# Kernel tuning notes

Measured on AMD Instinct MI355X. Metric: run time of the kernel, lower is better.

## Reference

```python
import jax, jax.numpy as jnp
import numpy as np

N_NODES = 50000
N_EDGES = 800000
D = 128


def setup_inputs() -> dict:
    key = jax.random.key(0)
    ks = jax.random.split(key, 8)
    s = 1.0 / np.sqrt(D)
    return {
        "x": jax.random.normal(ks[0], (N_NODES, D), dtype=jnp.float32),
        "edge_index": jax.random.randint(ks[1], (2, N_EDGES), 0, N_NODES, dtype=jnp.int32),
        "W0l": jax.random.normal(ks[2], (D, D), dtype=jnp.float32) * s,
        "b0l": jnp.zeros((D,), dtype=jnp.float32),
        "W0r": jax.random.normal(ks[3], (D, D), dtype=jnp.float32) * s,
        "W1l": jax.random.normal(ks[4], (D, D), dtype=jnp.float32) * s,
        "b1l": jnp.zeros((D,), dtype=jnp.float32),
        "W1r": jax.random.normal(ks[5], (D, D), dtype=jnp.float32) * s,
    }


def reference(x, edge_index, W0l, b0l, W0r, W1l, b1l, W1r):
    # Encoder(conv='sage', num_layers=2), eval mode (dropout = identity).
    src = edge_index[0]  # x_j gathered from source nodes
    dst = edge_index[1]  # aggregated at target nodes
    # in-degree for mean aggregation; isolated nodes get 0 aggregate (PyG mean)
    deg = jax.ops.segment_sum(jnp.ones_like(dst, dtype=x.dtype), dst, num_segments=N_NODES)
    inv_deg = jnp.where(deg > 0, 1.0 / jnp.maximum(deg, 1.0), 0.0)[:, None]

    def sage(h, Wl, bl, Wr):
        m = h @ Wl + bl                                        # lin_l
        agg = jax.ops.segment_sum(m[src], dst, num_segments=N_NODES) * inv_deg  # mean aggr
        return agg + h @ Wr                                    # + lin_r skip

    h = jax.nn.relu(sage(x, W0l, b0l, W0r))   # layer 0 + relu
    return sage(h, W1l, b1l, W1r)             # final layer
```

## Files before the change

kernel.cpp:

```cpp
#include <hip/hip_runtime.h>

#define N_NODES 50000
#define N_EDGES 800000
#define D 128
#define NBLK ((N_NODES + 255) / 256)
#define EPB 4096
#define CAP 8192
#define PCAP 8192

typedef __bf16 bf16x8 __attribute__((ext_vector_type(8)));
typedef short s16x8 __attribute__((ext_vector_type(8)));
typedef float f32x4 __attribute__((ext_vector_type(4)));
typedef float f32x2 __attribute__((ext_vector_type(2)));
typedef unsigned short u16;
typedef unsigned int u32;
typedef unsigned char u8;
typedef u32 u32x2 __attribute__((ext_vector_type(2)));
typedef u32 u32x4 __attribute__((ext_vector_type(4)));
typedef u16 u16x4 __attribute__((ext_vector_type(4)));

__device__ inline u16 f32_to_bf16(float f) {
    u32 u = __builtin_bit_cast(u32, f);
    u += 0x7fffu + ((u >> 16) & 1u);
    return (u16)(u >> 16);
}

__device__ inline f32x4 mfma16(s16x8 a, s16x8 b, f32x4 c) {
    return __builtin_amdgcn_mfma_f32_16x16x32_bf16(
        __builtin_bit_cast(bf16x8, a), __builtin_bit_cast(bf16x8, b), c, 0, 0, 0);
}

#define CAST_BLOCKS ((N_NODES * 16) / 256)
#define STAGE_BLOCKS ((N_EDGES + EPB - 1) / EPB)

__global__ __launch_bounds__(256) void prep_stage(
    const float* __restrict__ x, u16* __restrict__ xb, u16* __restrict__ hb,
    u8* __restrict__ xf8, u8* __restrict__ hf8,
    const float* __restrict__ W0l, const float* __restrict__ W0r,
    const float* __restrict__ W1l, const float* __restrict__ W1r,
    u16* __restrict__ Wp,
    const int* __restrict__ src, const int* __restrict__ dst,
    int* __restrict__ ccount, u32* __restrict__ staged) {
    __shared__ int hist[NBLK];
    __shared__ int base[NBLK];
    int t = threadIdx.x, b = blockIdx.x;
    if (b < CAST_BLOCKS) {
        int gid = b * 256 + t;
        const float* p = x + (size_t)gid * 8;
        f32x4 a = *(const f32x4*)p;
        f32x4 c = *(const f32x4*)(p + 4);
        u16 o[8];
#pragma unroll
        for (int j = 0; j < 4; j++) { o[j] = f32_to_bf16(a[j]); o[4 + j] = f32_to_bf16(c[j]); }
        *(s16x8*)(xb + (size_t)gid * 8) = *(const s16x8*)o;
        int p0 = __builtin_amdgcn_cvt_pk_fp8_f32(a.x, a.y, 0, false);
        int p1 = __builtin_amdgcn_cvt_pk_fp8_f32(a.z, a.w, 0, false);
        int p2 = __builtin_amdgcn_cvt_pk_fp8_f32(c.x, c.y, 0, false);
        int p3 = __builtin_amdgcn_cvt_pk_fp8_f32(c.z, c.w, 0, false);
        u32x2 w;
        w.x = (u32)(p0 & 0xffff) | ((u32)(p1 & 0xffff) << 16);
        w.y = (u32)(p2 & 0xffff) | ((u32)(p3 & 0xffff) << 16);
        *(u32x2*)(xf8 + (size_t)gid * 8) = w;
    } else if (b < CAST_BLOCKS + 32) {
        int gid = (b - CAST_BLOCKS) * 256 + t;
        int wsel = gid >> 11;
        int rem  = gid & 2047;
        int ct   = rem >> 8;
        int ks   = (rem >> 6) & 3;
        int lane = rem & 63;
        const float* W = (wsel == 0) ? W0l : (wsel == 1) ? W0r : (wsel == 2) ? W1l : W1r;
        int n  = ct * 16 + (lane & 15);
        int k0 = ks * 32 + (lane >> 4) * 8;
        u16 o[8];
#pragma unroll
        for (int j = 0; j < 8; j++) o[j] = f32_to_bf16(W[(k0 + j) * D + n]);
        u16* dp = Wp + wsel * 16384 + (size_t)((ct * 4 + ks) * 64 + lane) * 8;
        *(s16x8*)dp = *(const s16x8*)o;
    } else if (b < CAST_BLOCKS + 33) {
        if (t < 64)        ((u32*)(xb + (size_t)N_NODES * D))[t] = 0;
        else if (t < 128)  ((u32*)(hb + (size_t)N_NODES * D))[t - 64] = 0;
        else if (t < 160)  ((u32*)(xf8 + (size_t)N_NODES * D))[t - 128] = 0;
        else if (t < 192)  ((u32*)(hf8 + (size_t)N_NODES * D))[t - 160] = 0;
    } else {
        int sb = b - CAST_BLOCKS - 33;
        int bb = sb * EPB;
        if (t < NBLK) hist[t] = 0;
        __syncthreads();
        u32 pk[16]; int cb[16];
#pragma unroll
        for (int i = 0; i < 16; i++) {
            int e = bb + i * 256 + t;
            if (e < N_EDGES) {
                int sv = src[e], dv = dst[e];
                pk[i] = (u32)sv | ((u32)(dv & 255) << 16);
                cb[i] = dv >> 8;
                atomicAdd(&hist[cb[i]], 1);
            } else cb[i] = -1;
        }
        __syncthreads();
        if (t < NBLK) {
            int c = hist[t];
            if (c > 0) {
                int old = atomicAdd(&ccount[t], c);
                if (old > CAP - c) old = CAP - c;
                base[t] = t * CAP + old;
            }
            hist[t] = 0;
        }
        __syncthreads();
#pragma unroll
        for (int i = 0; i < 16; i++) {
            if (cb[i] >= 0) {
                int slot = atomicAdd(&hist[cb[i]], 1);
                staged[base[cb[i]] + slot] = pk[i];
            }
        }
    }
}

__global__ __launch_bounds__(256) void fine_kernel(const int* __restrict__ ccount,
                                                   const u32* __restrict__ staged,
                                                   u16* __restrict__ eidx,
                                                   u32* __restrict__ info,
                                                   float* __restrict__ inv) {
    __shared__ u32 sdata[CAP];
    __shared__ int hist[256];
    __shared__ int cursor[256];
    __shared__ int wsum[4];
    int t = threadIdx.x, cb = blockIdx.x;
    int lane = t & 63, wave = t >> 6;

    hist[t] = 0;
    __syncthreads();
    int c = ccount[cb];
    if (c > CAP) c = CAP;
    for (int i = t; i < c; i += 256) {
        u32 v = staged[cb * CAP + i];
        sdata[i] = v;
        atomicAdd(&hist[(v >> 16) & 255], 1);
    }
    __syncthreads();
    int d = hist[t];
    int pd = (d + 15) & ~15;
    int s = pd;
#pragma unroll
    for (int off = 1; off < 64; off <<= 1) {
        int u = __shfl_up(s, off, 64);
        if (lane >= off) s += u;
    }
    if (lane == 63) wsum[wave] = s;
    __syncthreads();
    int wadd = 0;
#pragma unroll
    for (int w = 0; w < 4; w++) if (w < wave) wadd += wsum[w];
    int gb = cb * PCAP + (s - pd + wadd);
    int node = cb * 256 + t;
    if (node < N_NODES) {
        info[node] = (u32)gb | ((u32)(pd >> 4) << 21);
        inv[node] = d > 0 ? 1.0f / (float)d : 0.0f;
    }
    cursor[t] = gb;
    __syncthreads();
    for (int i = t; i < c; i += 256) {
        u32 v = sdata[i];
        int pos = atomicAdd(&cursor[(v >> 16) & 255], 1);
        eidx[pos] = (u16)(v & 0xffffu);
    }
    for (int i = gb + d; i < gb + pd; i++) eidx[i] = (u16)N_NODES;
}

__device__ inline void issue_e(u16x4 (&e)[2], const u16* __restrict__ eidx,
                               const int (&basek)[2], const int (&rnds)[2],
                               int quad, int rr) {
#pragma unroll
    for (int k = 0; k < 2; k++)
        if (rr < rnds[k]) e[k] = *(const u16x4*)(eidx + basek[k] + rr * 16 + quad * 4);
}
__device__ inline void issue_g(u32x2 (&g)[2][4], const u16x4 (&e)[2],
                               const u8* __restrict__ AF8, const int (&rnds)[2],
                               int ql, int rr) {
#pragma unroll
    for (int k = 0; k < 2; k++)
        if (rr < rnds[k]) {
#pragma unroll
            for (int j = 0; j < 4; j++)
                g[k][j] = *(const u32x2*)(AF8 + (size_t)e[k][j] * D + ql * 8);
        }
}
__device__ inline void unpack_acc(f32x2 (&acc)[2][4], const u32x2 (&g)[2][4],
                                  const int (&rnds)[2], int rr) {
#pragma unroll
    for (int k = 0; k < 2; k++)
        if (rr < rnds[k]) {
#pragma unroll
            for (int j = 0; j < 4; j++) {
                u32x2 v = g[k][j];
                acc[k][0] += __builtin_amdgcn_cvt_pk_f32_fp8((int)v.x, false);
                acc[k][1] += __builtin_amdgcn_cvt_pk_f32_fp8((int)v.x, true);
                acc[k][2] += __builtin_amdgcn_cvt_pk_f32_fp8((int)v.y, false);
                acc[k][3] += __builtin_amdgcn_cvt_pk_f32_fp8((int)v.y, true);
            }
        }
}

template <int RELU, int OUTF32>
__global__ __launch_bounds__(512) void fused_layer(
    const u16* __restrict__ A, const u8* __restrict__ AF8,
    const u16* __restrict__ WpR, const u16* __restrict__ WpL,
    const float* __restrict__ bias, const float* __restrict__ inv,
    const u32* __restrict__ info, const u16* __restrict__ eidx,
    u16* __restrict__ outb, u8* __restrict__ outf8, float* __restrict__ outf) {
    __shared__ char mlds[16 * 256];
    int wave = threadIdx.x >> 6, lane = threadIdx.x & 63;
    int rowbase = blockIdx.x * 16;
    int quad = lane >> 4, ql = lane & 15;

    int basek[2], rnds[2];
#pragma unroll
    for (int k = 0; k < 2; k++) {
        u32 ifo = info[rowbase + wave * 2 + k];
        basek[k] = (int)(ifo & 0x1FFFFFu);
        rnds[k]  = (int)(ifo >> 21);
    }
    int maxr = rnds[0] > rnds[1] ? rnds[0] : rnds[1];

    f32x2 acc[2][4];
#pragma unroll
    for (int k = 0; k < 2; k++)
#pragma unroll
        for (int e = 0; e < 4; e++) acc[k][e] = (f32x2){0.f, 0.f};

    if (maxr > 0) {
        u16x4 eA[2], eB[2];
        u32x2 gA[2][4], gB[2][4];
        issue_e(eA, eidx, basek, rnds, quad, 0);
        issue_g(gA, eA, AF8, rnds, ql, 0);
        if (maxr > 1) issue_e(eB, eidx, basek, rnds, quad, 1);
        int r = 0;
        while (true) {
            if (r + 1 < maxr) issue_g(gB, eB, AF8, rnds, ql, r + 1);
            if (r + 2 < maxr) issue_e(eA, eidx, basek, rnds, quad, r + 2);
            unpack_acc(acc, gA, rnds, r);
            if (++r >= maxr) break;
            if (r + 1 < maxr) issue_g(gA, eA, AF8, rnds, ql, r + 1);
            if (r + 2 < maxr) issue_e(eB, eidx, basek, rnds, quad, r + 2);
            unpack_acc(acc, gB, rnds, r);
            if (++r >= maxr) break;
        }
    }

#pragma unroll
    for (int k = 0; k < 2; k++) {
        float v[8];
#pragma unroll
        for (int e = 0; e < 4; e++) { v[2 * e] = acc[k][e].x; v[2 * e + 1] = acc[k][e].y; }
#pragma unroll
        for (int j = 0; j < 8; j++) {
            v[j] += __shfl_xor(v[j], 16);
            v[j] += __shfl_xor(v[j], 32);
        }
        if (quad == 0) {
            int node = rowbase + wave * 2 + k;
            float iv = inv[node];
            u32x4 o;
            o.x = (u32)f32_to_bf16(v[0] * iv) | ((u32)f32_to_bf16(v[1] * iv) << 16);
            o.y = (u32)f32_to_bf16(v[2] * iv) | ((u32)f32_to_bf16(v[3] * iv) << 16);
            o.z = (u32)f32_to_bf16(v[4] * iv) | ((u32)f32_to_bf16(v[5] * iv) << 16);
            o.w = (u32)f32_to_bf16(v[6] * iv) | ((u32)f32_to_bf16(v[7] * iv) << 16);
            int lr = wave * 2 + k;
            *(u32x4*)(mlds + lr * 256 + ((ql ^ lr) & 15) * 16) = o;
        }
    }

    s16x8 bR[4], bL[4];
#pragma unroll
    for (int ks = 0; ks < 4; ks++) {
        size_t off = (size_t)((wave * 4 + ks) * 64 + lane) * 8;
        bR[ks] = *(const s16x8*)(WpR + off);
        bL[ks] = *(const s16x8*)(WpL + off);
    }
    __syncthreads();

    f32x4 acc2 = (f32x4){0.f, 0.f, 0.f, 0.f};
#pragma unroll
    for (int ks = 0; ks < 4; ks++) {
        s16x8 a1 = *(const s16x8*)(A + (size_t)(rowbase + ql) * D + ks * 32 + quad * 8);
        s16x8 a2 = *(const s16x8*)(mlds + ql * 256 + (((ks * 4 + quad) ^ ql) & 15) * 16);
        acc2 = mfma16(a1, bR[ks], acc2);
        acc2 = mfma16(a2, bL[ks], acc2);
    }

    float bv = bias[wave * 16 + ql];

#pragma unroll
    for (int i = 0; i < 4; i++) {
        int row = rowbase + quad * 4 + i;
        float mask = inv[row] > 0.f ? 1.f : 0.f;
        int col = wave * 16 + ql;
        float val = acc2[i] + mask * bv;
        if (RELU) val = val > 0.f ? val : 0.f;
        if (OUTF32) {
            outf[(size_t)row * D + col] = val;
        } else {
            outb[(size_t)row * D + col] = f32_to_bf16(val);
            int pk = __builtin_amdgcn_cvt_pk_fp8_f32(val, val, 0, false);
            outf8[(size_t)row * D + col] = (u8)(pk & 0xff);
        }
    }
}

extern "C" void kernel_launch(void* const* d_in, const int* in_sizes, int n_in,
                              void* d_out, int out_size, void* d_ws, size_t ws_size,
                              hipStream_t stream) {
    const float* x    = (const float*)d_in[0];
    const int*   edge = (const int*)d_in[1];
    const int*   src  = edge;
    const int*   dstn = edge + N_EDGES;
    const float* W0l  = (const float*)d_in[2];
    const float* b0l  = (const float*)d_in[3];
    const float* W0r  = (const float*)d_in[4];
    const float* W1l  = (const float*)d_in[5];
    const float* b1l  = (const float*)d_in[6];
    const float* W1r  = (const float*)d_in[7];
    float* out = (float*)d_out;

    char* p = (char*)d_ws;
    auto alloc = [&](size_t nb) { char* r = p; p += (nb + 255) & ~(size_t)255; return r; };
    int*   ccount = (int*)alloc((size_t)NBLK * 4);
    u32*   info   = (u32*)alloc((size_t)N_NODES * 4);
    float* inv    = (float*)alloc((size_t)N_NODES * 4);
    u32*   staged = (u32*)alloc((size_t)NBLK * CAP * 4);
    u16*   eidx   = (u16*)alloc((size_t)NBLK * PCAP * 2);
    u16*   xb     = (u16*)alloc((size_t)(N_NODES + 1) * D * 2);
    u16*   hb     = (u16*)alloc((size_t)(N_NODES + 1) * D * 2);
    u8*    xf8    = (u8*)alloc((size_t)(N_NODES + 1) * D);
    u8*    hf8    = (u8*)alloc((size_t)(N_NODES + 1) * D);
    u16*   Wp     = (u16*)alloc((size_t)4 * 16384 * 2);

    hipMemsetAsync(ccount, 0, (size_t)NBLK * 4, stream);

    prep_stage<<<CAST_BLOCKS + 33 + STAGE_BLOCKS, 256, 0, stream>>>(
        x, xb, hb, xf8, hf8, W0l, W0r, W1l, W1r, Wp, src, dstn, ccount, staged);
    fine_kernel<<<NBLK, 256, 0, stream>>>(ccount, staged, eidx, info, inv);

    int fblocks = N_NODES / 16;
    const u16* WpL0 = Wp;
    const u16* WpR0 = Wp + 16384;
    const u16* WpL1 = Wp + 2 * 16384;
    const u16* WpR1 = Wp + 3 * 16384;
    fused_layer<1, 0><<<fblocks, 512, 0, stream>>>(xb, xf8, WpR0, WpL0, b0l, inv, info, eidx, hb, hf8, nullptr);
    fused_layer<0, 1><<<fblocks, 512, 0, stream>>>(hb, hf8, WpR1, WpL1, b1l, inv, info, eidx, nullptr, nullptr, out);
}
```

Baseline: 206.1 us.

## Replace two-level bucketed CSR build with global degree histogram, scan, and atomic scatter

Rebuilds the CSR edge index construction: instead of staging edges into per-256-node buckets with shared-memory histograms and a per-bucket fine sort, it counts degrees with global atomics, does a block scan with an atomic global offset, and scatters source indices using per-node global atomic cursors. This removes the large staged buffer and the capacity-limited bucket passes, at the cost of one extra kernel launch, many contended global atomics, and a non-deterministic ordering of edges within each node's segment. It also drops the zero padding row for the bf16 buffers.

New measurement: 269.4 us. +30.7%, slower.

```diff
diff --git a/kernel.cpp b/kernel.cpp
--- a/kernel.cpp
+++ b/kernel.cpp
@@ -3,10 +3,7 @@
 #define N_NODES 50000
 #define N_EDGES 800000
 #define D 128
-#define NBLK ((N_NODES + 255) / 256)
-#define EPB 4096
-#define CAP 8192
-#define PCAP 8192
+#define PADMAX 1550000
 
 typedef __bf16 bf16x8 __attribute__((ext_vector_type(8)));
 typedef short s16x8 __attribute__((ext_vector_type(8)));
@@ -31,18 +28,15 @@
 }
 
 #define CAST_BLOCKS ((N_NODES * 16) / 256)
-#define STAGE_BLOCKS ((N_EDGES + EPB - 1) / EPB)
+#define HIST_BLOCKS ((N_EDGES + 2047) / 2048)
 
 __global__ __launch_bounds__(256) void prep_stage(
-    const float* __restrict__ x, u16* __restrict__ xb, u16* __restrict__ hb,
+    const float* __restrict__ x, u16* __restrict__ xb,
     u8* __restrict__ xf8, u8* __restrict__ hf8,
     const float* __restrict__ W0l, const float* __restrict__ W0r,
     const float* __restrict__ W1l, const float* __restrict__ W1r,
     u16* __restrict__ Wp,
-    const int* __restrict__ src, const int* __restrict__ dst,
-    int* __restrict__ ccount, u32* __restrict__ staged) {
-    __shared__ int hist[NBLK];
-    __shared__ int base[NBLK];
+    const int* __restrict__ dst, int* __restrict__ deg) {
     int t = threadIdx.x, b = blockIdx.x;
     if (b < CAST_BLOCKS) {
         int gid = b * 256 + t;
@@ -77,70 +71,32 @@
         u16* dp = Wp + wsel * 16384 + (size_t)((ct * 4 + ks) * 64 + lane) * 8;
         *(s16x8*)dp = *(const s16x8*)o;
     } else if (b < CAST_BLOCKS + 33) {
-        if (t < 64)        ((u32*)(xb + (size_t)N_NODES * D))[t] = 0;
-        else if (t < 128)  ((u32*)(hb + (size_t)N_NODES * D))[t - 64] = 0;
-        else if (t < 160)  ((u32*)(xf8 + (size_t)N_NODES * D))[t - 128] = 0;
-        else if (t < 192)  ((u32*)(hf8 + (size_t)N_NODES * D))[t - 160] = 0;
+        if (t < 32)       ((u32*)(xf8 + (size_t)N_NODES * D))[t] = 0;
+        else if (t < 64)  ((u32*)(hf8 + (size_t)N_NODES * D))[t - 32] = 0;
     } else {
         int sb = b - CAST_BLOCKS - 33;
-        int bb = sb * EPB;
-        if (t < NBLK) hist[t] = 0;
-        __syncthreads();
-        u32 pk[16]; int cb[16];
-#pragma unroll
-        for (int i = 0; i < 16; i++) {
-            int e = bb + i * 256 + t;
-            if (e < N_EDGES) {
-                int sv = src[e], dv = dst[e];
-                pk[i] = (u32)sv | ((u32)(dv & 255) << 16);
-                cb[i] = dv >> 8;
-                atomicAdd(&hist[cb[i]], 1);
-            } else cb[i] = -1;
-        }
-        __syncthreads();
-        if (t < NBLK) {
-            int c = hist[t];
-            if (c > 0) {
-                int old = atomicAdd(&ccount[t], c);
-                if (old > CAP - c) old = CAP - c;
-                base[t] = t * CAP + old;
-            }
-            hist[t] = 0;
-        }
-        __syncthreads();
-#pragma unroll
-        for (int i = 0; i < 16; i++) {
-            if (cb[i] >= 0) {
-                int slot = atomicAdd(&hist[cb[i]], 1);
-                staged[base[cb[i]] + slot] = pk[i];
-            }
-        }
-    }
-}
-
-__global__ __launch_bounds__(256) void fine_kernel(const int* __restrict__ ccount,
-                                                   const u32* __restrict__ staged,
-                                                   u16* __restrict__ eidx,
-                                                   u32* __restrict__ info,
-                                                   float* __restrict__ inv) {
-    __shared__ u32 sdata[CAP];
-    __shared__ int hist[256];
-    __shared__ int cursor[256];
+        int i0 = sb * 2048 + t * 8;
+        if (i0 < N_EDGES) {
+            u32x4 d0 = *(const u32x4*)(dst + i0);
+            u32x4 d1 = *(const u32x4*)(dst + i0 + 4);
+            atomicAdd(&deg[(int)d0.x], 1); atomicAdd(&deg[(int)d0.y], 1);
+            atomicAdd(&deg[(int)d0.z], 1); atomicAdd(&deg[(int)d0.w], 1);
+            atomicAdd(&deg[(int)d1.x], 1); atomicAdd(&deg[(int)d1.y], 1);
+            atomicAdd(&deg[(int)d1.z], 1); atomicAdd(&deg[(int)d1.w], 1);
+        }
+    }
+}
+
+__global__ __launch_bounds__(256) void scan_kernel(
+    const int* __restrict__ deg, int* __restrict__ total,
+    u32* __restrict__ info, float* __restrict__ inv,
+    int* __restrict__ cursor, u16* __restrict__ eidx) {
     __shared__ int wsum[4];
-    int t = threadIdx.x, cb = blockIdx.x;
+    __shared__ int gbase;
+    int t = threadIdx.x, b = blockIdx.x;
     int lane = t & 63, wave = t >> 6;
-
-    hist[t] = 0;
-    __syncthreads();
-    int c = ccount[cb];
-    if (c > CAP) c = CAP;
-    for (int i = t; i < c; i += 256) {
-        u32 v = staged[cb * CAP + i];
-        sdata[i] = v;
-        atomicAdd(&hist[(v >> 16) & 255], 1);
-    }
-    __syncthreads();
-    int d = hist[t];
+    int n = b * 256 + t;
+    int d = (n < N_NODES) ? deg[n] : 0;
     int pd = (d + 15) & ~15;
     int s = pd;
 #pragma unroll
@@ -150,23 +106,38 @@
     }
     if (lane == 63) wsum[wave] = s;
     __syncthreads();
+    if (t == 0) gbase = atomicAdd(total, wsum[0] + wsum[1] + wsum[2] + wsum[3]);
+    __syncthreads();
     int wadd = 0;
 #pragma unroll
     for (int w = 0; w < 4; w++) if (w < wave) wadd += wsum[w];
-    int gb = cb * PCAP + (s - pd + wadd);
-    int node = cb * 256 + t;
-    if (node < N_NODES) {
-        info[node] = (u32)gb | ((u32)(pd >> 4) << 21);
-        inv[node] = d > 0 ? 1.0f / (float)d : 0.0f;
-    }
-    cursor[t] = gb;
-    __syncthreads();
-    for (int i = t; i < c; i += 256) {
-        u32 v = sdata[i];
-        int pos = atomicAdd(&cursor[(v >> 16) & 255], 1);
-        eidx[pos] = (u16)(v & 0xffffu);
-    }
-    for (int i = gb + d; i < gb + pd; i++) eidx[i] = (u16)N_NODES;
+    int gb = gbase + (s - pd) + wadd;
+    if (n < N_NODES) {
+        info[n] = (u32)gb | ((u32)(pd >> 4) << 21);
+        inv[n] = d > 0 ? 1.0f / (float)d : 0.0f;
+        cursor[n] = gb;
+        for (int i = gb + d; i < gb + pd; i++) eidx[i] = (u16)N_NODES;
+    }
+}
+
+__global__ __launch_bounds__(256) void scatter_kernel(
+    const int* __restrict__ src, const int* __restrict__ dst,
+    int* __restrict__ cursor, u16* __restrict__ eidx) {
+    int i0 = blockIdx.x * 2048 + threadIdx.x * 8;
+    if (i0 >= N_EDGES) return;
+    u32x4 s0 = *(const u32x4*)(src + i0);
+    u32x4 s1 = *(const u32x4*)(src + i0 + 4);
+    u32x4 d0 = *(const u32x4*)(dst + i0);
+    u32x4 d1 = *(const u32x4*)(dst + i0 + 4);
+    int sv[8] = {(int)s0.x, (int)s0.y, (int)s0.z, (int)s0.w,
+                 (int)s1.x, (int)s1.y, (int)s1.z, (int)s1.w};
+    int dv[8] = {(int)d0.x, (int)d0.y, (int)d0.z, (int)d0.w,
+                 (int)d1.x, (int)d1.y, (int)d1.z, (int)d1.w};
+#pragma unroll
+    for (int j = 0; j < 8; j++) {
+        int pos = atomicAdd(&cursor[dv[j]], 1);
+        eidx[pos] = (u16)sv[j];
+    }
 }
 
 __device__ inline void issue_e(u16x4 (&e)[2], const u16* __restrict__ eidx,
@@ -326,22 +297,24 @@
 
     char* p = (char*)d_ws;
     auto alloc = [&](size_t nb) { char* r = p; p += (nb + 255) & ~(size_t)255; return r; };
-    int*   ccount = (int*)alloc((size_t)NBLK * 4);
+    int*   deg    = (int*)alloc((size_t)(N_NODES + 1) * 4);
     u32*   info   = (u32*)alloc((size_t)N_NODES * 4);
     float* inv    = (float*)alloc((size_t)N_NODES * 4);
-    u32*   staged = (u32*)alloc((size_t)NBLK * CAP * 4);
-    u16*   eidx   = (u16*)alloc((size_t)NBLK * PCAP * 2);
-    u16*   xb     = (u16*)alloc((size_t)(N_NODES + 1) * D * 2);
-    u16*   hb     = (u16*)alloc((size_t)(N_NODES + 1) * D * 2);
+    int*   cursor = (int*)alloc((size_t)N_NODES * 4);
+    u16*   eidx   = (u16*)alloc((size_t)PADMAX * 2);
+    u16*   xb     = (u16*)alloc((size_t)N_NODES * D * 2);
+    u16*   hb     = (u16*)alloc((size_t)N_NODES * D * 2);
     u8*    xf8    = (u8*)alloc((size_t)(N_NODES + 1) * D);
     u8*    hf8    = (u8*)alloc((size_t)(N_NODES + 1) * D);
     u16*   Wp     = (u16*)alloc((size_t)4 * 16384 * 2);
-
-    hipMemsetAsync(ccount, 0, (size_t)NBLK * 4, stream);
-
-    prep_stage<<<CAST_BLOCKS + 33 + STAGE_BLOCKS, 256, 0, stream>>>(
-        x, xb, hb, xf8, hf8, W0l, W0r, W1l, W1r, Wp, src, dstn, ccount, staged);
-    fine_kernel<<<NBLK, 256, 0, stream>>>(ccount, staged, eidx, info, inv);
+    int*   total  = deg + N_NODES;
+
+    hipMemsetAsync(deg, 0, (size_t)(N_NODES + 1) * 4, stream);
+
+    prep_stage<<<CAST_BLOCKS + 33 + HIST_BLOCKS, 256, 0, stream>>>(
+        x, xb, xf8, hf8, W0l, W0r, W1l, W1r, Wp, dstn, deg);
+    scan_kernel<<<(N_NODES + 255) / 256, 256, 0, stream>>>(deg, total, info, inv, cursor, eidx);
+    scatter_kernel<<<HIST_BLOCKS, 256, 0, stream>>>(src, dstn, cursor, eidx);
 
     int fblocks = N_NODES / 16;
     const u16* WpL0 = Wp;
```
